# Kernel optimization log

Hardware: AMD Instinct MI355X
Metric: run time of the kernel (lower is better)

Reference implementation:

```python
import jax, jax.numpy as jnp
import numpy as np

N = 16384          # number of input points
K = 16             # kNN neighbors for EdgeConv
SCALES = (4096, 1024, 256)
DIM = 256
EC_HID = 64        # EdgeConv output dim
MLP_HID = 128


def _sqdist(a, b):
    # squared euclidean distance matrix: (Na, Nb)
    return (jnp.sum(a * a, axis=1, keepdims=True)
            - 2.0 * (a @ b.T)
            + jnp.sum(b * b, axis=1)[None, :])


def _fps(points, n):
    # farthest point sampling, deterministic start at index 0
    d = jnp.sum((points - points[0]) ** 2, axis=1)  # (N,)

    def step(d, _):
        nxt = jnp.argmax(d)
        d = jnp.minimum(d, jnp.sum((points - points[nxt]) ** 2, axis=1))
        return d, nxt

    _, rest = jax.lax.scan(step, d, None, length=n - 1)
    return jnp.concatenate([jnp.zeros((1,), dtype=rest.dtype), rest])


def setup_inputs() -> dict:
    key = jax.random.key(0)
    ks = jax.random.split(key, 10)

    def lin(k, fi, fo):
        return (jax.random.normal(k, (fi, fo), jnp.float32) / np.sqrt(fi)).astype(jnp.float32)

    nsc = len(SCALES)
    return {
        "points": jax.random.normal(ks[0], (N, 3), jnp.float32),
        # EdgeConv MLP: Linear(6,64) -> ReLU -> Linear(64,64)
        "ew1": lin(ks[1], 6, EC_HID), "eb1": jnp.zeros((EC_HID,), jnp.float32),
        "ew2": lin(ks[2], EC_HID, EC_HID), "eb2": jnp.zeros((EC_HID,), jnp.float32),
        # per-scale MLPs: Linear(64,128) -> ReLU -> Linear(128,256), stacked over scales
        "mw1": jnp.stack([lin(jax.random.fold_in(ks[3], i), EC_HID, MLP_HID) for i in range(nsc)]),
        "mb1": jnp.zeros((nsc, MLP_HID), jnp.float32),
        "mw2": jnp.stack([lin(jax.random.fold_in(ks[4], i), MLP_HID, DIM) for i in range(nsc)]),
        "mb2": jnp.zeros((nsc, DIM), jnp.float32),
    }


def _edge_conv(points, ew1, eb1, ew2, eb2):
    # kNN graph (loop=False): exclude self via +inf diagonal; indices not differentiated
    d = jax.lax.stop_gradient(_sqdist(points, points))
    d = d.at[jnp.arange(N), jnp.arange(N)].set(jnp.inf)
    _, idx = jax.lax.top_k(-d, K)                      # (N, K) neighbor indices
    x_i = points[:, None, :]                           # (N, 1, 3) centers
    x_j = points[idx]                                  # (N, K, 3) neighbors
    ef = jnp.concatenate([jnp.broadcast_to(x_i, (N, K, 3)), x_j - x_i], axis=-1)  # (N,K,6)
    h = jax.nn.relu(ef @ ew1 + eb1) @ ew2 + eb2        # (N, K, 64)
    # scatter_max over centers == max over the K neighbor axis (every center has K edges)
    return jnp.max(h, axis=1)                          # (N, 64)


def reference(points, ew1, eb1, ew2, eb2, mw1, mb1, mw2, mb2):
    feats = _edge_conv(points, ew1, eb1, ew2, eb2)     # (N, 64)
    outs = []
    prev_pts = None
    for i, scale in enumerate(SCALES):
        if i == 0:
            fi = _fps(points, scale)
            sp = points[fi]
            sf = feats[fi]
        else:
            fi = _fps(prev_pts, scale)
            sp = prev_pts[fi]
            nn = jnp.argmin(_sqdist(sp, points), axis=1)  # nearest source point per query
            sf = feats[nn]
        lf = jax.nn.relu(sf @ mw1[i] + mb1[i]) @ mw2[i] + mb2[i]  # (scale, DIM)
        outs.append(sp)
        outs.append(lf)
        prev_pts = sp
    return tuple(outs)
```

## Files before the change

kernel.cpp:

```cpp
#include <hip/hip_runtime.h>
#include <cfloat>
#include <cstdint>

#define N_PTS 16384
#define KNN_K 16
#define KNN_TILE 512
#define CERT_EPS 3e-6f

struct FpsSmem {
    float sx[N_PTS];
    unsigned long long slots[2][16];
    int cw2[2][2];
    float4 pub;
    int cand_idx[64];
    int cand_cnt;
    int more_flag;
    double red_d[16];
};

template <int CTRL>
__device__ __forceinline__ unsigned dpp_mov_u32(unsigned v) {
    return (unsigned)__builtin_amdgcn_update_dpp((int)v, (int)v, CTRL, 0xF, 0xF, false);
}

__device__ __forceinline__ void cross_slot_reduce(unsigned long long k, float& M1, int& G1) {
    unsigned hi = (unsigned)(k >> 32), lo = (unsigned)k;
#define RSTEP(CTRL)                                          \
    {                                                        \
        const unsigned ohi = dpp_mov_u32<CTRL>(hi);          \
        const unsigned olo = dpp_mov_u32<CTRL>(lo);          \
        const bool b = (ohi > hi) || (ohi == hi && olo > lo);\
        hi = b ? ohi : hi;                                   \
        lo = b ? olo : lo;                                   \
    }
    RSTEP(0x121)
    RSTEP(0x122)
    RSTEP(0x124)
    RSTEP(0x128)
#undef RSTEP
    M1 = __uint_as_float(hi);
    G1 = (int)(~lo);
}

__device__ __forceinline__ void fps_run(FpsSmem& sm, const float* __restrict__ pts,
                                        int n_out, int* __restrict__ fi) {
    constexpr int T = 1024;
    constexpr int P = 16;
    constexpr int NW = T / 64;
    const int tid = threadIdx.x;
    const int wave = tid >> 6, lane = tid & 63;

    if (tid < 32) sm.slots[tid >> 4][tid & 15] = 0ull;
    if (tid < 4) sm.cw2[tid >> 1][tid & 1] = 0;

    float yr[P], zr[P], c[P];
    const float sx0 = pts[0], sy0 = pts[1], sz0 = pts[2];
    if (tid == 0) fi[0] = 0;

    float m1 = -1.0f, m2 = -1.0f;
    int g1 = 0x7fffffff;
#pragma unroll
    for (int q = 0; q < P; ++q) {
        const int g = tid + q * T;
        const float x = pts[g * 3 + 0];
        const float y = pts[g * 3 + 1];
        const float z = pts[g * 3 + 2];
        sm.sx[g] = x;
        yr[q] = y;
        zr[q] = z;
        const float dx = x - sx0, dy = y - sy0, dz = z - sz0;
        const float t = fmaf(dx, dx, fmaf(dy, dy, dz * dz));
        const float nc = fminf(FLT_MAX, t);
        c[q] = nc;
        const bool gt = nc > m1;
        m2 = fmaxf(m2, fminf(nc, m1));
        m1 = fmaxf(m1, nc);
        g1 = gt ? g : g1;
    }
    __syncthreads();
    {
        const unsigned long long key =
            ((unsigned long long)__float_as_uint(m1) << 32) |
            (unsigned long long)(~(unsigned)g1);
        atomicMax(&sm.slots[1][tid & 15], key);
    }

    for (int s = 1; s < n_out; ++s) {
        __syncthreads();
        const int par = s & 1;

        const unsigned long long k0 = sm.slots[par][lane & 15];
        float M1;
        int G1;
        cross_slot_reduce(k0, M1, G1);
        const float thr = M1 - M1 * CERT_EPS;

        if (g1 == G1) {
            const int qw = (G1 - tid) >> 10;
            float yw = 0.0f, zw = 0.0f;
#pragma unroll
            for (int q = 0; q < P; ++q)
                if (q == qw) { yw = yr[q]; zw = zr[q]; }
            sm.pub = make_float4(sm.sx[G1], yw, zw, 0.0f);
        }

        if (tid < 16) sm.slots[par ^ 1][tid] = 0ull;
        if (tid == 0) { sm.cw2[par ^ 1][0] = 0; sm.cw2[par ^ 1][1] = 0; }

        const unsigned long long bal = __ballot(m1 >= thr);
        if (lane == 0) atomicAdd(&sm.cw2[par][0], (int)__popcll(bal));
        if (g1 == G1) sm.cw2[par][1] = (m2 >= thr) ? 1 : 0;

        __syncthreads();
        const int2 tw = *reinterpret_cast<const int2*>(&sm.cw2[par][0]);
        const int total = tw.x, wfl = tw.y;
        const float4 wc = sm.pub;
        float nx = wc.x, ny = wc.y, nz = wc.z;
        int wg = G1;

        if (total > 1 || wfl) {
            unsigned miss = 0;
#pragma unroll
            for (int q = 0; q < P; ++q)
                if (c[q] >= thr) miss |= (1u << q);
            double BD = -1.0;
            int BG = 0x7fffffff;
            for (;;) {
                if (tid == 0) { sm.cand_cnt = 0; sm.more_flag = 0; }
                __syncthreads();
#pragma unroll
                for (int q = 0; q < P; ++q) {
                    if (miss & (1u << q)) {
                        int slot = atomicAdd(&sm.cand_cnt, 1);
                        if (slot < 64) {
                            sm.cand_idx[slot] = tid + q * T;
                            miss &= ~(1u << q);
                        } else {
                            sm.more_flag = 1;
                        }
                    }
                }
                __syncthreads();
                int ncand = sm.cand_cnt;
                if (ncand > 64) ncand = 64;
                for (int ci = 0; ci < ncand; ++ci) {
                    const int g = sm.cand_idx[ci];
                    const double qx = (double)pts[g * 3 + 0];
                    const double qy = (double)pts[g * 3 + 1];
                    const double qz = (double)pts[g * 3 + 2];
                    double dmin = DBL_MAX;
                    for (int i = tid; i < s; i += T) {
                        const int h = fi[i];
                        double ddx = qx - (double)pts[h * 3 + 0];
                        double ddy = qy - (double)pts[h * 3 + 1];
                        double ddz = qz - (double)pts[h * 3 + 2];
                        double dd = ddx * ddx + ddy * ddy + ddz * ddz;
                        dmin = (dd < dmin) ? dd : dmin;
                    }
                    for (int off = 32; off; off >>= 1) {
                        double od = __shfl_xor(dmin, off);
                        dmin = (od < dmin) ? od : dmin;
                    }
                    if (lane == 0) sm.red_d[wave] = dmin;
                    __syncthreads();
                    double dall = sm.red_d[0];
#pragma unroll
                    for (int w = 1; w < NW; ++w) dall = (sm.red_d[w] < dall) ? sm.red_d[w] : dall;
                    if (dall > BD || (dall == BD && g < BG)) { BD = dall; BG = g; }
                    __syncthreads();
                }
                int mf = sm.more_flag;
                __syncthreads();
                if (!mf) break;
            }
            wg = BG;
            nx = pts[wg * 3 + 0];
            ny = pts[wg * 3 + 1];
            nz = pts[wg * 3 + 2];
        }

        if (tid == 0) fi[s] = wg;
        if (s == n_out - 1) break;

        float nm1 = -1.0f, nm2 = -1.0f;
        int ng1 = 0x7fffffff;
#pragma unroll
        for (int q = 0; q < P; ++q) {
            const float dx = sm.sx[tid + q * T] - nx;
            const float dy = yr[q] - ny, dz = zr[q] - nz;
            const float t = fmaf(dx, dx, fmaf(dy, dy, dz * dz));
            const float nc = fminf(c[q], t);
            c[q] = nc;
            const bool gt = nc > nm1;
            nm2 = fmaxf(nm2, fminf(nc, nm1));
            nm1 = fmaxf(nm1, nc);
            ng1 = gt ? (tid + q * T) : ng1;
        }
        m1 = nm1; m2 = nm2; g1 = ng1;
        const unsigned long long key =
            ((unsigned long long)__float_as_uint(m1) << 32) |
            (unsigned long long)(~(unsigned)g1);
        atomicMax(&sm.slots[par ^ 1][tid & 15], key);
    }
}

struct KnnSmem {
    float sx[KNN_TILE], sy[KNN_TILE], sz[KNN_TILE];
    float w1[6 * 64], b1v[64], w2[64 * 64], b2v[64];
};

__device__ __forceinline__ void knn_edge_body(
    KnnSmem& sm, const float* __restrict__ pts,
    const float* __restrict__ ew1, const float* __restrict__ eb1,
    const float* __restrict__ ew2, const float* __restrict__ eb2,
    float* __restrict__ feats, int qb) {
    for (int t = threadIdx.x; t < 6 * 64; t += 1024) sm.w1[t] = ew1[t];
    for (int t = threadIdx.x; t < 64; t += 1024) { sm.b1v[t] = eb1[t]; sm.b2v[t] = eb2[t]; }
    for (int t = threadIdx.x; t < 64 * 64; t += 1024) sm.w2[t] = ew2[t];

    const int wave = threadIdx.x >> 6;
    const int lane = threadIdx.x & 63;
    const int qi = qb * 16 + wave;
    const double qxd = (double)pts[qi * 3 + 0];
    const double qyd = (double)pts[qi * 3 + 1];
    const double qzd = (double)pts[qi * 3 + 2];

    double ld[16];
    int li[16];
#pragma unroll
    for (int s = 0; s < 16; ++s) { ld[s] = DBL_MAX; li[s] = 0x7fffffff; }
    double md = DBL_MAX; int mj = 0x7fffffff; int mslot = 0;

    for (int t0 = 0; t0 < N_PTS; t0 += KNN_TILE) {
        __syncthreads();
        for (int t = threadIdx.x; t < KNN_TILE; t += 1024) {
            sm.sx[t] = pts[(t0 + t) * 3 + 0];
            sm.sy[t] = pts[(t0 + t) * 3 + 1];
            sm.sz[t] = pts[(t0 + t) * 3 + 2];
        }
        __syncthreads();
#pragma unroll
        for (int m = 0; m < KNN_TILE / 64; ++m) {
            const int cc = lane + m * 64;
            const int j = t0 + cc;
            if (j == qi) continue;
            double dx = qxd - (double)sm.sx[cc];
            double dy = qyd - (double)sm.sy[cc];
            double dz = qzd - (double)sm.sz[cc];
            double dd = dx * dx + dy * dy + dz * dz;
            if (dd < md || (dd == md && j < mj)) {
#pragma unroll
                for (int s = 0; s < 16; ++s)
                    if (s == mslot) { ld[s] = dd; li[s] = j; }
                md = -1.0; mj = -1; mslot = 0;
#pragma unroll
                for (int s = 0; s < 16; ++s) {
                    bool g = (ld[s] > md) || (ld[s] == md && li[s] > mj);
                    if (g) { md = ld[s]; mj = li[s]; mslot = s; }
                }
            }
        }
    }

    const float xi = pts[qi * 3], yi = pts[qi * 3 + 1], zi = pts[qi * 3 + 2];
    float acc = -FLT_MAX;
    for (int r = 0; r < KNN_K; ++r) {
        double cd = DBL_MAX; int cj = 0x7fffffff; int cs = 0;
#pragma unroll
        for (int s = 0; s < 16; ++s) {
            bool l = (ld[s] < cd) || (ld[s] == cd && li[s] < cj);
            if (l) { cd = ld[s]; cj = li[s]; cs = s; }
        }
        double wd = cd; int wj = cj;
        for (int off = 32; off; off >>= 1) {
            double od = __shfl_xor(wd, off);
            int oj = __shfl_xor(wj, off);
            if (od < wd || (od == wd && oj < wj)) { wd = od; wj = oj; }
        }
        if (cd == wd && cj == wj) {
#pragma unroll
            for (int s = 0; s < 16; ++s)
                if (s == cs) { ld[s] = DBL_MAX; li[s] = 0x7fffffff; }
        }
        const float xj = pts[wj * 3], yj = pts[wj * 3 + 1], zj = pts[wj * 3 + 2];
        const float f3 = xj - xi, f4 = yj - yi, f5 = zj - zi;
        float h1 = sm.b1v[lane];
        h1 = fmaf(xi, sm.w1[0 * 64 + lane], h1);
        h1 = fmaf(yi, sm.w1[1 * 64 + lane], h1);
        h1 = fmaf(zi, sm.w1[2 * 64 + lane], h1);
        h1 = fmaf(f3, sm.w1[3 * 64 + lane], h1);
        h1 = fmaf(f4, sm.w1[4 * 64 + lane], h1);
        h1 = fmaf(f5, sm.w1[5 * 64 + lane], h1);
        h1 = fmaxf(h1, 0.0f);
        float h2 = sm.b2v[lane];
        for (int d = 0; d < 64; ++d)
            h2 = fmaf(__shfl(h1, d), sm.w2[d * 64 + lane], h2);
        acc = fmaxf(acc, h2);
    }
    feats[qi * 64 + lane] = acc;
}

__global__ __launch_bounds__(1024)
void mega_kernel(const float* __restrict__ pts,
                 const float* __restrict__ ew1, const float* __restrict__ eb1,
                 const float* __restrict__ ew2, const float* __restrict__ eb2,
                 float* __restrict__ feats,
                 int* __restrict__ fi0,
                 float* __restrict__ sp0, float* __restrict__ sp1,
                 float* __restrict__ sp2) {
    constexpr size_t SMEM_BYTES =
        sizeof(FpsSmem) > sizeof(KnnSmem) ? sizeof(FpsSmem) : sizeof(KnnSmem);
    __shared__ __align__(16) char raw[SMEM_BYTES];
    if (blockIdx.x == 0) {
        FpsSmem& sm = *reinterpret_cast<FpsSmem*>(raw);
        fps_run(sm, pts, 4096, fi0);
        __syncthreads();
        const int tid = threadIdx.x;
        for (int t = tid; t < 4096; t += 1024) {
            const int g = fi0[t];
            const float x = pts[g * 3 + 0];
            const float y = pts[g * 3 + 1];
            const float z = pts[g * 3 + 2];
            sp0[t * 3 + 0] = x;
            sp0[t * 3 + 1] = y;
            sp0[t * 3 + 2] = z;
            if (t < 1024) {
                sp1[t * 3 + 0] = x;
                sp1[t * 3 + 1] = y;
                sp1[t * 3 + 2] = z;
            }
            if (t < 256) {
                sp2[t * 3 + 0] = x;
                sp2[t * 3 + 1] = y;
                sp2[t * 3 + 2] = z;
            }
        }
    } else {
        knn_edge_body(*reinterpret_cast<KnnSmem*>(raw), pts, ew1, eb1, ew2, eb2,
                      feats, blockIdx.x - 1);
    }
}

__device__ __forceinline__ void mlp_body(
    const float* __restrict__ feats, const int* __restrict__ orig,
    const float* __restrict__ mw1, const float* __restrict__ mb1,
    const float* __restrict__ mw2, const float* __restrict__ mb2,
    float* __restrict__ outp, int pb) {
    __shared__ float sfl[64], h1l[128];
    const int t = threadIdx.x;
    for (int pl = 0; pl < 16; ++pl) {
        const int p = pb * 16 + pl;
        const int g = orig[p];
        if (t < 64) sfl[t] = feats[g * 64 + t];
        __syncthreads();
        if (t < 128) {
            float h = mb1[t];
            for (int dd = 0; dd < 64; ++dd)
                h = fmaf(sfl[dd], mw1[dd * 128 + t], h);
            h1l[t] = fmaxf(h, 0.0f);
        }
        __syncthreads();
        float o = mb2[t];
        for (int dd = 0; dd < 128; ++dd)
            o = fmaf(h1l[dd], mw2[dd * 256 + t], o);
        outp[p * 256 + t] = o;
        __syncthreads();
    }
}

__global__ __launch_bounds__(256) void tail_kernel(
    const float* __restrict__ feats,
    const int* __restrict__ fi0,
    const float* __restrict__ mw1, const float* __restrict__ mb1,
    const float* __restrict__ mw2, const float* __restrict__ mb2,
    float* __restrict__ out) {
    const int b = blockIdx.x;
    float* lf0 = out + 12288;
    float* lf1 = out + 1063936;
    float* lf2 = out + 1326848;
    if (b < 256) {
        mlp_body(feats, fi0, mw1 + 0 * 8192, mb1 + 0 * 128,
                 mw2 + 0 * 32768, mb2 + 0 * 256, lf0, b);
    } else if (b < 320) {
        mlp_body(feats, fi0, mw1 + 1 * 8192, mb1 + 1 * 128,
                 mw2 + 1 * 32768, mb2 + 1 * 256, lf1, b - 256);
    } else {
        mlp_body(feats, fi0, mw1 + 2 * 8192, mb1 + 2 * 128,
                 mw2 + 2 * 32768, mb2 + 2 * 256, lf2, b - 320);
    }
}

extern "C" void kernel_launch(void* const* d_in, const int* in_sizes, int n_in,
                              void* d_out, int out_size, void* d_ws, size_t ws_size,
                              hipStream_t stream) {
    const float* pts = (const float*)d_in[0];
    const float* ew1 = (const float*)d_in[1];
    const float* eb1 = (const float*)d_in[2];
    const float* ew2 = (const float*)d_in[3];
    const float* eb2 = (const float*)d_in[4];
    const float* mw1 = (const float*)d_in[5];
    const float* mb1 = (const float*)d_in[6];
    const float* mw2 = (const float*)d_in[7];
    const float* mb2 = (const float*)d_in[8];
    float* out = (float*)d_out;
    char* ws = (char*)d_ws;

    float* feats = (float*)(ws + 0);
    int* fi0 = (int*)(ws + 4194304);

    float* sp0 = out + 0;
    float* sp1 = out + 1060864;
    float* sp2 = out + 1326080;

    mega_kernel<<<1 + N_PTS / 16, 1024, 0, stream>>>(pts, ew1, eb1, ew2, eb2, feats,
                                                     fi0, sp0, sp1, sp2);
    tail_kernel<<<336, 256, 0, stream>>>(feats, fi0, mw1, mb1, mw2, mb2, out);
}
```

Before: 7.461 ms.

## Replace FPS atomic slot reduction with wave-level DPP top-2 and single barrier

The FPS loop now reduces max and second-max within each wave using DPP row and broadcast steps. Each wave posts one key plus its m2 to shared memory, and a final 16-way DPP reduce runs after one barrier. This removes the atomicMax/atomicAdd counters, the winner publish step and the second __syncthreads per iteration, and reads the winner coordinates from shared sx/sy and global z. It also keeps x in registers, and the EdgeConv second layer reads h1 through shared memory as float4 instead of 64 shuffles. The cost is more registers and shared memory.

```diff
diff --git a/kernel.cpp b/kernel.cpp
--- a/kernel.cpp
+++ b/kernel.cpp
@@ -9,9 +9,9 @@
 
 struct FpsSmem {
     float sx[N_PTS];
-    unsigned long long slots[2][16];
-    int cw2[2][2];
-    float4 pub;
+    float sy[N_PTS];
+    unsigned long long skey[2][16];
+    float sm2v[2][16];
     int cand_idx[64];
     int cand_cnt;
     int more_flag;
@@ -23,23 +23,32 @@
     return (unsigned)__builtin_amdgcn_update_dpp((int)v, (int)v, CTRL, 0xF, 0xF, false);
 }
 
-__device__ __forceinline__ void cross_slot_reduce(unsigned long long k, float& M1, int& G1) {
-    unsigned hi = (unsigned)(k >> 32), lo = (unsigned)k;
-#define RSTEP(CTRL)                                          \
-    {                                                        \
-        const unsigned ohi = dpp_mov_u32<CTRL>(hi);          \
-        const unsigned olo = dpp_mov_u32<CTRL>(lo);          \
-        const bool b = (ohi > hi) || (ohi == hi && olo > lo);\
-        hi = b ? ohi : hi;                                   \
-        lo = b ? olo : lo;                                   \
-    }
-    RSTEP(0x121)
-    RSTEP(0x122)
-    RSTEP(0x124)
-    RSTEP(0x128)
-#undef RSTEP
-    M1 = __uint_as_float(hi);
-    G1 = (int)(~lo);
+template <int CTRL>
+__device__ __forceinline__ void top2_step(unsigned& hi, unsigned& lo, float& m2) {
+    const unsigned ohi = dpp_mov_u32<CTRL>(hi);
+    const unsigned olo = dpp_mov_u32<CTRL>(lo);
+    const float om2 = __uint_as_float(dpp_mov_u32<CTRL>(__float_as_uint(m2)));
+    const bool sw = (ohi > hi) || (ohi == hi && olo > lo);
+    const float lm1 = __uint_as_float(sw ? hi : ohi);
+    m2 = fmaxf(sw ? om2 : m2, lm1);
+    hi = sw ? ohi : hi;
+    lo = sw ? olo : lo;
+}
+
+__device__ __forceinline__ void wave_post_top2(FpsSmem& sm, int p, int wave, int lane,
+                                               float m1, float m2, int g1) {
+    unsigned hi = __float_as_uint(m1);
+    unsigned lo = ~(unsigned)g1;
+    top2_step<0x121>(hi, lo, m2);
+    top2_step<0x122>(hi, lo, m2);
+    top2_step<0x124>(hi, lo, m2);
+    top2_step<0x128>(hi, lo, m2);
+    top2_step<0x142>(hi, lo, m2);
+    top2_step<0x143>(hi, lo, m2);
+    if (lane == 63) {
+        sm.skey[p][wave] = ((unsigned long long)hi << 32) | (unsigned long long)lo;
+        sm.sm2v[p][wave] = m2;
+    }
 }
 
 __device__ __forceinline__ void fps_run(FpsSmem& sm, const float* __restrict__ pts,
@@ -50,10 +59,7 @@
     const int tid = threadIdx.x;
     const int wave = tid >> 6, lane = tid & 63;
 
-    if (tid < 32) sm.slots[tid >> 4][tid & 15] = 0ull;
-    if (tid < 4) sm.cw2[tid >> 1][tid & 1] = 0;
-
-    float yr[P], zr[P], c[P];
+    float xr[P], yr[P], zr[P], c[P];
     const float sx0 = pts[0], sy0 = pts[1], sz0 = pts[2];
     if (tid == 0) fi[0] = 0;
 
@@ -66,8 +72,8 @@
         const float y = pts[g * 3 + 1];
         const float z = pts[g * 3 + 2];
         sm.sx[g] = x;
-        yr[q] = y;
-        zr[q] = z;
+        sm.sy[g] = y;
+        xr[q] = x; yr[q] = y; zr[q] = z;
         const float dx = x - sx0, dy = y - sy0, dz = z - sz0;
         const float t = fmaf(dx, dx, fmaf(dy, dy, dz * dz));
         const float nc = fminf(FLT_MAX, t);
@@ -77,48 +83,34 @@
         m1 = fmaxf(m1, nc);
         g1 = gt ? g : g1;
     }
-    __syncthreads();
-    {
-        const unsigned long long key =
-            ((unsigned long long)__float_as_uint(m1) << 32) |
-            (unsigned long long)(~(unsigned)g1);
-        atomicMax(&sm.slots[1][tid & 15], key);
-    }
+    wave_post_top2(sm, 1, wave, lane, m1, m2, g1);
 
     for (int s = 1; s < n_out; ++s) {
         __syncthreads();
         const int par = s & 1;
 
-        const unsigned long long k0 = sm.slots[par][lane & 15];
-        float M1;
-        int G1;
-        cross_slot_reduce(k0, M1, G1);
+        unsigned hi, lo;
+        float M2v;
+        {
+            const unsigned long long k0 = sm.skey[par][lane & 15];
+            M2v = sm.sm2v[par][lane & 15];
+            hi = (unsigned)(k0 >> 32);
+            lo = (unsigned)k0;
+            top2_step<0x121>(hi, lo, M2v);
+            top2_step<0x122>(hi, lo, M2v);
+            top2_step<0x124>(hi, lo, M2v);
+            top2_step<0x128>(hi, lo, M2v);
+        }
+        const float M1 = __uint_as_float(hi);
+        const int G1 = (int)(~lo);
         const float thr = M1 - M1 * CERT_EPS;
 
-        if (g1 == G1) {
-            const int qw = (G1 - tid) >> 10;
-            float yw = 0.0f, zw = 0.0f;
-#pragma unroll
-            for (int q = 0; q < P; ++q)
-                if (q == qw) { yw = yr[q]; zw = zr[q]; }
-            sm.pub = make_float4(sm.sx[G1], yw, zw, 0.0f);
-        }
-
-        if (tid < 16) sm.slots[par ^ 1][tid] = 0ull;
-        if (tid == 0) { sm.cw2[par ^ 1][0] = 0; sm.cw2[par ^ 1][1] = 0; }
-
-        const unsigned long long bal = __ballot(m1 >= thr);
-        if (lane == 0) atomicAdd(&sm.cw2[par][0], (int)__popcll(bal));
-        if (g1 == G1) sm.cw2[par][1] = (m2 >= thr) ? 1 : 0;
-
-        __syncthreads();
-        const int2 tw = *reinterpret_cast<const int2*>(&sm.cw2[par][0]);
-        const int total = tw.x, wfl = tw.y;
-        const float4 wc = sm.pub;
-        float nx = wc.x, ny = wc.y, nz = wc.z;
+        float nx = sm.sx[G1];
+        float ny = sm.sy[G1];
+        float nz = pts[G1 * 3 + 2];
         int wg = G1;
 
-        if (total > 1 || wfl) {
+        if (M2v >= thr) {
             unsigned miss = 0;
 #pragma unroll
             for (int q = 0; q < P; ++q)
@@ -186,8 +178,7 @@
         int ng1 = 0x7fffffff;
 #pragma unroll
         for (int q = 0; q < P; ++q) {
-            const float dx = sm.sx[tid + q * T] - nx;
-            const float dy = yr[q] - ny, dz = zr[q] - nz;
+            const float dx = xr[q] - nx, dy = yr[q] - ny, dz = zr[q] - nz;
             const float t = fmaf(dx, dx, fmaf(dy, dy, dz * dz));
             const float nc = fminf(c[q], t);
             c[q] = nc;
@@ -197,16 +188,14 @@
             ng1 = gt ? (tid + q * T) : ng1;
         }
         m1 = nm1; m2 = nm2; g1 = ng1;
-        const unsigned long long key =
-            ((unsigned long long)__float_as_uint(m1) << 32) |
-            (unsigned long long)(~(unsigned)g1);
-        atomicMax(&sm.slots[par ^ 1][tid & 15], key);
+        wave_post_top2(sm, par ^ 1, wave, lane, m1, m2, g1);
     }
 }
 
 struct KnnSmem {
     float sx[KNN_TILE], sy[KNN_TILE], sz[KNN_TILE];
     float w1[6 * 64], b1v[64], w2[64 * 64], b2v[64];
+    __align__(16) float h1buf[16][64];
 };
 
 __device__ __forceinline__ void knn_edge_body(
@@ -292,9 +281,17 @@
         h1 = fmaf(f4, sm.w1[4 * 64 + lane], h1);
         h1 = fmaf(f5, sm.w1[5 * 64 + lane], h1);
         h1 = fmaxf(h1, 0.0f);
+        sm.h1buf[wave][lane] = h1;
         float h2 = sm.b2v[lane];
-        for (int d = 0; d < 64; ++d)
-            h2 = fmaf(__shfl(h1, d), sm.w2[d * 64 + lane], h2);
+        const float4* h4 = reinterpret_cast<const float4*>(&sm.h1buf[wave][0]);
+#pragma unroll
+        for (int dd = 0; dd < 16; ++dd) {
+            const float4 hv = h4[dd];
+            h2 = fmaf(hv.x, sm.w2[(dd * 4 + 0) * 64 + lane], h2);
+            h2 = fmaf(hv.y, sm.w2[(dd * 4 + 1) * 64 + lane], h2);
+            h2 = fmaf(hv.z, sm.w2[(dd * 4 + 2) * 64 + lane], h2);
+            h2 = fmaf(hv.w, sm.w2[(dd * 4 + 3) * 64 + lane], h2);
+        }
         acc = fmaxf(acc, h2);
     }
     feats[qi * 64 + lane] = acc;
```

Result: slower. 9.754 ms (+30.7%).
